# Kernel tuning notes

Measured on AMD Instinct MI355X. Metric: run time of the kernel, lower is better.

Reference implementation:

```python
import jax, jax.numpy as jnp
import numpy as np
from jax import lax

BN_EPS = 1e-5
EYE_EPS = 1e-6
ZIP = 128
TAU = 0.2

def _cov(x):
    # x: [C, N] rows=variables, cols=observations (torch.cov semantics)
    n = x.shape[1]
    xc = x - jnp.mean(x, axis=1, keepdims=True)
    return (xc @ xc.T) / (n - 1)

def setup_inputs() -> dict:
    key = jax.random.key(0)
    ks = jax.random.split(key, 10)
    d = {}
    d["img_feats_f"] = jax.random.normal(ks[0], (1, 128, 480, 640), dtype=jnp.float32)
    d["pcd_feats_f"] = jax.random.normal(ks[1], (22432, 128), dtype=jnp.float32)
    # ConvBlock(128->128, k=3, s=1, p=1) + BatchNorm (eval) + ReLU
    d["conv_w"] = jax.random.normal(ks[2], (128, 128, 3, 3), dtype=jnp.float32) * 0.02
    d["conv_b"] = jnp.zeros((128,), dtype=jnp.float32)
    d["bn_gamma"] = jnp.ones((128,), dtype=jnp.float32)
    d["bn_beta"] = jnp.zeros((128,), dtype=jnp.float32)
    d["bn_mean"] = jnp.zeros((128,), dtype=jnp.float32)
    d["bn_var"] = jnp.ones((128,), dtype=jnp.float32)
    # Linear(128->128) + ReLU
    d["lin_w"] = jax.random.normal(ks[3], (128, 128), dtype=jnp.float32) * 0.02
    d["lin_b"] = jnp.zeros((128,), dtype=jnp.float32)
    return d

def reference(img_feats_f, pcd_feats_f, conv_w, conv_b, bn_gamma, bn_beta, bn_mean, bn_var, lin_w, lin_b):
    B, C, h, w = img_feats_f.shape
    # zip_fea_2d: Conv2d(3x3, pad 1) + BN(eval) + ReLU
    x = lax.conv_general_dilated(img_feats_f, conv_w, (1, 1), ((1, 1), (1, 1)),
                                 dimension_numbers=("NCHW", "OIHW", "NCHW"))
    x = x + conv_b[None, :, None, None]
    x = (x - bn_mean[None, :, None, None]) * (bn_gamma / jnp.sqrt(bn_var + BN_EPS))[None, :, None, None] + bn_beta[None, :, None, None]
    img_zip = jax.nn.relu(x)
    # zip_fea_3d: Linear + ReLU
    pcd_zip = jax.nn.relu(pcd_feats_f @ lin_w.T + lin_b)

    tmp_img_f = img_zip.reshape(ZIP, -1)        # [128, h*w]
    tmp_pcd_f = pcd_zip.T                        # [128, Np]
    cov_img = _cov(tmp_img_f)                    # [128, 128]
    cov_pcd = _cov(tmp_pcd_f)                    # [128, 128]

    eye = jnp.eye(ZIP, dtype=cov_img.dtype) * EYE_EPS
    sc_ip = (cov_img @ jnp.linalg.inv(cov_pcd + eye)) / ZIP
    sc_pi = (cov_pcd @ jnp.linalg.inv(cov_img + eye)) / ZIP
    at_ip = jax.nn.softmax(sc_pi, axis=-1)
    at_pi = jax.nn.softmax(sc_ip, axis=-1)
    tmp_img_fb = (at_ip @ tmp_img_f).reshape(-1, h, w)[None]   # [1,128,h,w]
    tmp_pcd_fb = (at_pi @ tmp_pcd_f).T                          # [Np,128]

    at_ii = jax.nn.softmax((cov_img @ cov_img.T) / ZIP, axis=-1)
    at_pp = jax.nn.softmax((cov_pcd @ cov_pcd.T) / ZIP, axis=-1)
    tmp_img_fa = (at_ii @ tmp_img_f).reshape(-1, h, w)[None]
    tmp_pcd_fa = (at_pp @ tmp_pcd_f).T

    img_out = (tmp_img_fb + tmp_img_fa) / 2 * TAU + img_feats_f * (1 - TAU)
    pcd_out = (tmp_pcd_fb + tmp_pcd_fa) / 2 * TAU + pcd_feats_f * (1 - TAU)
    return (img_out, pcd_out)
```

## Files before the change

### kernel.cpp

```cpp
#include <hip/hip_runtime.h>
#include <math.h>

#define HH 480
#define WW 640
#define HWSZ (HH*WW)
#define NPC 22432
#define IMG_SZ (128*HWSZ)
#define NBI 256
#define NBP 64
#define CHUNK_I 1200
#define CHUNK_P 351

typedef unsigned short u16;
typedef unsigned int u32;
typedef __attribute__((ext_vector_type(8))) short bf16x8;
typedef __attribute__((ext_vector_type(4))) float f32x4;

#define OFF_SUMS_IMG 0
#define OFF_SUMS_PCD 128
#define OFF_BIAS2    256
#define OFF_COV_IMG  512
#define OFF_COV_PCD  16896
#define OFF_INV_IMG  33280
#define OFF_INV_PCD  49664
#define OFF_MT_IMG   66048
#define OFF_MT_PCD   82432
#define OFF_LWT      98816
#define OFF_PSUMS    115200
#define OFF_MB       147968
#define OFF_WT       152064
#define OFF_PSUMS_P  OFF_WT
#define OFF_PART_IMG 299520
#define OFF_PART_PCD 4493824
#define OFF_WB       5542400
#define OFF_TIMG_F   5616128
#define TIMG_PAD_W 642
#define TIMG_PX (482*642)
#define TIMG_PLANE (TIMG_PX*32)
#define WS_NEED_FLOATS 25420544

__device__ inline u32 pack_bf16(float a, float b) {
  u32 ua = __float_as_uint(a), ub = __float_as_uint(b);
  ua += 0x7FFFu + ((ua >> 16) & 1u);
  ub += 0x7FFFu + ((ub >> 16) & 1u);
  return (ua >> 16) | (ub & 0xFFFF0000u);
}
__device__ inline u16 to_bf16(float v) {
  u32 u = __float_as_uint(v); u += 0x7FFFu + ((u >> 16) & 1u);
  return (u16)(u >> 16);
}
__device__ inline float4 f4_fnma(float4 v, float f, float4 p) {
  return make_float4(v.x - f*p.x, v.y - f*p.y, v.z - f*p.z, v.w - f*p.w);
}

__global__ void prep_kernel(const float* __restrict__ conv_w, const float* __restrict__ conv_b,
                            const float* __restrict__ gamma, const float* __restrict__ beta,
                            const float* __restrict__ mean, const float* __restrict__ var,
                            const float* __restrict__ lin_w, float* __restrict__ ws, int big) {
  int tid = blockIdx.x * blockDim.x + threadIdx.x;
  int nth = gridDim.x * blockDim.x;
  for (int oc = tid; oc < 128; oc += nth) {
    float s = gamma[oc] / sqrtf(var[oc] + 1e-5f);
    ws[OFF_BIAS2 + oc] = (conv_b[oc] - mean[oc]) * s + beta[oc];
  }
  if (big) {
    u16* Wf = (u16*)(ws + OFF_WB);
    for (int e = tid; e < 9*128*128; e += nth) {
      int j = e & 7, l = (e >> 3) & 63, ob = (e >> 9) & 7;
      int ci32 = (e >> 12) & 3, tap = e >> 14;
      int oc = ob*16 + (l & 15);
      int ci = ci32*32 + ((l >> 4) & 3)*8 + j;
      float s = gamma[oc] / sqrtf(var[oc] + 1e-5f);
      Wf[e] = to_bf16(conv_w[(oc*128 + ci)*9 + tap] * s);
    }
  } else {
    for (int e = tid; e < 128*9*128; e += nth) {
      int oc = e & 127; int k = (e >> 7) % 9; int ci = e / 1152;
      float s = gamma[oc] / sqrtf(var[oc] + 1e-5f);
      ws[OFF_WT + e] = conv_w[(oc*128 + ci)*9 + k] * s;
    }
  }
  for (int e = tid; e < 128*128; e += nth) {
    int c2 = e & 127; int k = e >> 7;
    ws[OFF_LWT + e] = lin_w[c2*128 + k];
  }
}

__launch_bounds__(256)
__global__ void timg_kernel(const float* __restrict__ img, u16* __restrict__ Timg) {
  __shared__ float xt[64][133];
  const int b = blockIdx.x;
  const int t = threadIdx.x;
  if (b >= 4800) {
    int tid = (b - 4800) * 256 + t;
    if (tid < (642*2 + 480*2) * 16) {
      int px = tid >> 4, u = tid & 15;
      int q = u >> 2, j = u & 3;
      int addr;
      if (px < 642) addr = px;
      else if (px < 1284) addr = 481*642 + (px - 642);
      else if (px < 1764) addr = (px - 1284 + 1) * 642;
      else addr = (px - 1764 + 1) * 642 + 641;
      ((uint4*)Timg)[(size_t)q*(TIMG_PX*4) + (size_t)addr*4 + j] = make_uint4(0u,0u,0u,0u);
    }
    return;
  }
  const int h = b / 10, w0 = (b % 10) * 64;
  const int wq = t & 15, cg = t >> 4;
#pragma unroll
  for (int i = 0; i < 8; ++i) {
    int ci = cg + i*16;
    float4 v = *(const float4*)&img[(size_t)ci*HWSZ + h*WW + w0 + wq*4];
    xt[wq*4+0][ci] = v.x; xt[wq*4+1][ci] = v.y;
    xt[wq*4+2][ci] = v.z; xt[wq*4+3][ci] = v.w;
  }
  __syncthreads();
  const int wp = t >> 2, q = t & 3, c0 = q * 32;
  u32 out[16];
#pragma unroll
  for (int j = 0; j < 16; ++j) {
    float a = xt[wp][c0 + 2*j], bb = xt[wp][c0 + 2*j + 1];
    out[j] = pack_bf16(a, bb);
  }
  u16* dst = Timg + (size_t)q*TIMG_PLANE
           + ((size_t)(h+1)*TIMG_PAD_W + (w0 + 1 + wp)) * 32;
#pragma unroll
  for (int qq = 0; qq < 4; ++qq)
    *(uint4*)(dst + qq*8) = make_uint4(out[qq*4], out[qq*4+1], out[qq*4+2], out[qq*4+3]);
}

#define REG_ROWS 6
#define REG_COLS 66
#define REG_PX (REG_ROWS*REG_COLS)
__launch_bounds__(256, 2)
__global__ void conv_mfma6_kernel(const u16* __restrict__ Timg,
                                  const u16* __restrict__ Wf,
                                  const float* __restrict__ ws,
                                  float* __restrict__ X) {
  __shared__ __align__(16) u16 reg_lds[REG_PX * 44];
  const int b = blockIdx.x;
  const int h0 = (b / 10) * 4;
  const int w0 = (b % 10) * 64;
  const int t = threadIdx.x;
  const int wv = t >> 6, l = t & 63;
  const int n_lane = l & 15, k_lane = l >> 4;
  const int ocg = wv & 1;
  const int rowg = wv >> 1;

  f32x4 acc[4][8];
#pragma unroll
  for (int mt = 0; mt < 4; ++mt)
#pragma unroll
    for (int nt = 0; nt < 8; ++nt) acc[mt][nt] = (f32x4){0.f,0.f,0.f,0.f};

#pragma unroll 1
  for (int qc = 0; qc < 4; ++qc) {
    __syncthreads();
    const u16* plane = Timg + (size_t)qc * TIMG_PLANE;
    for (int e = t; e < REG_PX * 4; e += 256) {
      int px = e >> 2, j = e & 3;
      int r = px / REG_COLS, c = px - r * REG_COLS;
      const u16* src = plane + ((size_t)(h0 + r) * TIMG_PAD_W + (w0 + c)) * 32 + j*8;
      *(uint4*)((char*)reg_lds + px * 88 + j * 16) = *(const uint4*)src;
    }
    __syncthreads();
    const u16* wq = Wf + (qc*8 + ocg*4)*512 + l*8;
#pragma unroll 1
    for (int tap = 0; tap < 9; ++tap) {
      const int kh = (tap * 11) >> 5;
      const int kw = tap - kh * 3;
      const int cb = n_lane + kw;
      const int rb = rowg*2 + kh;
      const u16* wtap = wq + tap * 16384;
      bf16x8 Af[4], Bf[8];
#pragma unroll
      for (int mt = 0; mt < 4; ++mt)
        Af[mt] = *(const bf16x8*)(wtap + mt*512);
#pragma unroll
      for (int nt = 0; nt < 8; ++nt) {
        int px = (rb + (nt >> 2)) * REG_COLS + cb + (nt & 3) * 16;
        Bf[nt] = *(const bf16x8*)((char*)reg_lds + px * 88 + k_lane * 16);
      }
#pragma unroll
      for (int mt = 0; mt < 4; ++mt)
#pragma unroll
        for (int nt = 0; nt < 8; ++nt)
          acc[mt][nt] = __builtin_amdgcn_mfma_f32_16x16x32_bf16(Af[mt], Bf[nt], acc[mt][nt], 0, 0, 0);
    }
  }
  const float* bias = ws + OFF_BIAS2;
#pragma unroll
  for (int mt = 0; mt < 4; ++mt) {
    f32x4 bv = *(const f32x4*)(bias + ocg*64 + mt*16 + k_lane*4);
#pragma unroll
    for (int nt = 0; nt < 8; ++nt) {
      int row = h0 + rowg*2 + (nt >> 2);
      int col = w0 + (nt & 3)*16 + n_lane;
#pragma unroll
      for (int rr = 0; rr < 4; ++rr) {
        int oc = ocg*64 + mt*16 + k_lane*4 + rr;
        float v = acc[mt][nt][rr] + bv[rr];
        X[(size_t)oc * HWSZ + row*WW + col] = fmaxf(v, 0.f);
      }
    }
  }
}

__launch_bounds__(256)
__global__ void conv_kernel(const float* __restrict__ img,
                            const float* __restrict__ ws,
                            float* __restrict__ outX) {
  __shared__ __align__(16) float xs[8][10][20];
  __shared__ __align__(16) float wsm[8][9][64];
  const int b = blockIdx.x;
  const int oc0 = (b & 1) * 64;
  const int sidx = b >> 1;
  const int h0 = (sidx / 40) * 8;
  const int w0 = (sidx % 40) * 16;
  const int t = threadIdx.x;
  const int oc_t = t & 15;
  const int px_t = t >> 4;
  const int ph = px_t >> 1;
  const int pw0 = (px_t & 1) * 8;
  float acc[4][8];
#pragma unroll
  for (int o = 0; o < 4; o++)
#pragma unroll
    for (int m = 0; m < 8; m++) acc[o][m] = 0.f;
  const float* wT = ws + OFF_WT;
  for (int ci0 = 0; ci0 < 128; ci0 += 8) {
    __syncthreads();
    for (int e = t; e < 1440; e += 256) {
      int ci = e / 180; int rem = e - ci*180; int r = rem / 18; int cc2 = rem - r*18;
      int gh = h0 + r - 1, gw = w0 + cc2 - 1;
      float v = 0.f;
      if ((unsigned)gh < (unsigned)HH && (unsigned)gw < (unsigned)WW)
        v = img[(ci0+ci)*HWSZ + gh*WW + gw];
      xs[ci][r][cc2] = v;
    }
    for (int e = t; e < 4608; e += 256) {
      int oc = e & 63; int k = (e >> 6) % 9; int ci = e / 576;
      wsm[ci][k][oc] = wT[((ci0+ci)*9 + k)*128 + oc0 + oc];
    }
    __syncthreads();
#pragma unroll
    for (int ci = 0; ci < 8; ci++) {
#pragma unroll
      for (int kh = 0; kh < 3; kh++) {
        float x10[10];
        float4 xa = *(const float4*)&xs[ci][ph+kh][pw0];
        float4 xb = *(const float4*)&xs[ci][ph+kh][pw0+4];
        x10[0]=xa.x; x10[1]=xa.y; x10[2]=xa.z; x10[3]=xa.w;
        x10[4]=xb.x; x10[5]=xb.y; x10[6]=xb.z; x10[7]=xb.w;
        x10[8]=xs[ci][ph+kh][pw0+8]; x10[9]=xs[ci][ph+kh][pw0+9];
#pragma unroll
        for (int kw = 0; kw < 3; kw++) {
          float4 wv = *(const float4*)&wsm[ci][kh*3+kw][oc_t*4];
#pragma unroll
          for (int m = 0; m < 8; m++) {
            float xv = x10[kw+m];
            acc[0][m] += wv.x*xv; acc[1][m] += wv.y*xv;
            acc[2][m] += wv.z*xv; acc[3][m] += wv.w*xv;
          }
        }
      }
    }
  }
#pragma unroll
  for (int o = 0; o < 4; o++) {
    int oc = oc0 + oc_t*4 + o;
    float bias = ws[OFF_BIAS2 + oc];
    float4 r0, r1;
    r0.x = fmaxf(acc[o][0]+bias, 0.f); r0.y = fmaxf(acc[o][1]+bias, 0.f);
    r0.z = fmaxf(acc[o][2]+bias, 0.f); r0.w = fmaxf(acc[o][3]+bias, 0.f);
    r1.x = fmaxf(acc[o][4]+bias, 0.f); r1.y = fmaxf(acc[o][5]+bias, 0.f);
    r1.z = fmaxf(acc[o][6]+bias, 0.f); r1.w = fmaxf(acc[o][7]+bias, 0.f);
    float* dst = outX + (size_t)oc*HWSZ + (h0+ph)*WW + w0 + pw0;
    *(float4*)dst = r0; *(float4*)(dst+4) = r1;
  }
}

__launch_bounds__(256)
__global__ void linear_kernel(const float* __restrict__ pcd,
                              const float* __restrict__ ws,
                              const float* __restrict__ lin_b,
                              float* __restrict__ Z) {
  __shared__ __align__(16) float Mt[128][132];
  __shared__ __align__(16) float zs[16][132];
  const int b = blockIdx.x, t = threadIdx.x;
  const int n0 = b * 16;
#pragma unroll
  for (int i = 0; i < 16; i++) {
    int idx = t + i*256; int r = idx >> 5; int c4 = (idx & 31)*4;
    *(float4*)&Mt[r][c4] = *(const float4*)&ws[OFF_LWT + r*128 + c4];
  }
#pragma unroll
  for (int i = 0; i < 2; i++) {
    int idx = t + i*256; int r = idx >> 5; int c4 = (idx & 31)*4;
    *(float4*)&zs[r][c4] = *(const float4*)&pcd[(size_t)(n0+r)*128 + c4];
  }
  __syncthreads();
  const int nl = t & 15;
  const int c0 = (t >> 4) * 8;
  float acc[8];
#pragma unroll
  for (int q = 0; q < 8; q++) acc[q] = 0.f;
#pragma unroll 8
  for (int k = 0; k < 128; k++) {
    float z = zs[nl][k];
    float4 wa = *(const float4*)&Mt[k][c0];
    float4 wb = *(const float4*)&Mt[k][c0+4];
    acc[0]+=z*wa.x; acc[1]+=z*wa.y; acc[2]+=z*wa.z; acc[3]+=z*wa.w;
    acc[4]+=z*wb.x; acc[5]+=z*wb.y; acc[6]+=z*wb.z; acc[7]+=z*wb.w;
  }
  float4 ba = *(const float4*)&lin_b[c0];
  float4 bb = *(const float4*)&lin_b[c0+4];
  float4 r0, r1;
  r0.x = fmaxf(acc[0]+ba.x,0.f); r0.y = fmaxf(acc[1]+ba.y,0.f);
  r0.z = fmaxf(acc[2]+ba.z,0.f); r0.w = fmaxf(acc[3]+ba.w,0.f);
  r1.x = fmaxf(acc[4]+bb.x,0.f); r1.y = fmaxf(acc[5]+bb.y,0.f);
  r1.z = fmaxf(acc[6]+bb.z,0.f); r1.w = fmaxf(acc[7]+bb.w,0.f);
  float* dst = Z + (size_t)(n0+nl)*128 + c0;
  *(float4*)dst = r0; *(float4*)(dst+4) = r1;
}

__launch_bounds__(256)
__global__ void gram_img_mfma_kernel(const float* __restrict__ X,
                                     float* __restrict__ part,
                                     float* __restrict__ psums) {
  __shared__ __align__(16) u16 tile[128*64];
  const int b = blockIdx.x, t = threadIdx.x;
  const int px0 = b * CHUNK_I;
  const int pg = t & 15;
  const int g0 = t >> 4;
  const int wv = t >> 6, l = t & 63;
  const int i0 = (wv >> 1) * 64, j0 = (wv & 1) * 64;
  const int row16 = l & 15, kq = l >> 4;
  float csum[8];
#pragma unroll
  for (int q = 0; q < 8; ++q) csum[q] = 0.f;
  f32x4 acc[4][4];
#pragma unroll
  for (int a = 0; a < 4; ++a)
#pragma unroll
    for (int q = 0; q < 4; ++q) acc[a][q] = (f32x4){0.f,0.f,0.f,0.f};

  for (int ti = 0; ti < 19; ++ti) {
    const int plg = ti*64 + pg*4;
    float4 v[8];
    if (ti < 18) {
#pragma unroll
      for (int cc = 0; cc < 8; ++cc) {
        int c = g0 + cc*16;
        v[cc] = *(const float4*)(X + (size_t)c*HWSZ + px0 + plg);
      }
    } else {
#pragma unroll
      for (int cc = 0; cc < 8; ++cc) {
        int c = g0 + cc*16;
        const float* src = X + (size_t)c*HWSZ + px0;
#pragma unroll
        for (int j = 0; j < 4; ++j) {
          int p = plg + j;
          ((float*)&v[cc])[j] = (p < CHUNK_I) ? src[p] : 0.f;
        }
      }
    }
    __syncthreads();
#pragma unroll
    for (int cc = 0; cc < 8; ++cc) {
      int c = g0 + cc*16;
      csum[cc] += v[cc].x + v[cc].y + v[cc].z + v[cc].w;
      u32 w0 = pack_bf16(v[cc].x, v[cc].y);
      u32 w1 = pack_bf16(v[cc].z, v[cc].w);
      *(uint2*)((char*)tile + c*128 + ((pg*8) ^ ((c & 7) << 4))) = make_uint2(w0, w1);
    }
    __syncthreads();
#pragma unroll
    for (int f = 0; f < 2; ++f) {
      bf16x8 Af[4], Bf[4];
#pragma unroll
      for (int mt = 0; mt < 4; ++mt) {
        int c = i0 + mt*16 + row16;
        Af[mt] = *(const bf16x8*)((char*)tile + c*128 + ((f*64 + kq*16) ^ ((c & 7) << 4)));
      }
#pragma unroll
      for (int nt = 0; nt < 4; ++nt) {
        int c = j0 + nt*16 + row16;
        Bf[nt] = *(const bf16x8*)((char*)tile + c*128 + ((f*64 + kq*16) ^ ((c & 7) << 4)));
      }
#pragma unroll
      for (int mt = 0; mt < 4; ++mt)
#pragma unroll
        for (int nt = 0; nt < 4; ++nt)
          acc[mt][nt] = __builtin_amdgcn_mfma_f32_16x16x32_bf16(Af[mt], Bf[nt], acc[mt][nt], 0, 0, 0);
    }
  }
#pragma unroll
  for (int cc = 0; cc < 8; ++cc) {
    float s = csum[cc];
    s += __shfl_xor(s, 1, 64);
    s += __shfl_xor(s, 2, 64);
    s += __shfl_xor(s, 4, 64);
    s += __shfl_xor(s, 8, 64);
    if (pg == 0) psums[b*128 + g0 + cc*16] = s;
  }
  float* dst = part + (size_t)b*16384;
#pragma unroll
  for (int mt = 0; mt < 4; ++mt)
#pragma unroll
    for (int nt = 0; nt < 4; ++nt) {
#pragma unroll
      for (int r = 0; r < 4; ++r) {
        int i = i0 + mt*16 + kq*4 + r;
        int j = j0 + nt*16 + row16;
        dst[i*128 + j] = acc[mt][nt][r];
      }
    }
}

__launch_bounds__(256)
__global__ void gram_pcd_kernel(const float* __restrict__ Z, float* __restrict__ part,
                                float* __restrict__ psums_p) {
  __shared__ __align__(16) float zt[64][132];
  __shared__ float ps4[4][32][4];
  const int b = blockIdx.x, t = threadIdx.x;
  const int n0 = b * CHUNK_P;
  const int i0 = (t >> 4) * 8, j0 = (t & 15) * 8;
  float acc[8][8];
#pragma unroll
  for (int a = 0; a < 8; a++)
#pragma unroll
    for (int q = 0; q < 8; q++) acc[a][q] = 0.f;
  float fsum[4] = {0.f, 0.f, 0.f, 0.f};
  for (int tile = 0; tile < 6; tile++) {
    __syncthreads();
#pragma unroll
    for (int i = 0; i < 8; i++) {
      int idx = t + i*256; int r = idx >> 5; int c4 = (idx & 31)*4;
      int lrow = tile*64 + r;
      int n = n0 + lrow;
      float4 v = {0.f,0.f,0.f,0.f};
      if (lrow < CHUNK_P && n < NPC) v = *(const float4*)&Z[(size_t)n*128 + c4];
      *(float4*)&zt[r][c4] = v;
      fsum[0] += v.x; fsum[1] += v.y; fsum[2] += v.z; fsum[3] += v.w;
    }
    __syncthreads();
#pragma unroll 4
    for (int n = 0; n < 64; n++) {
      float4 a0 = *(const float4*)&zt[n][i0];
      float4 a1 = *(const float4*)&zt[n][i0+4];
      float4 b0 = *(const float4*)&zt[n][j0];
      float4 b1 = *(const float4*)&zt[n][j0+4];
      float av[8] = {a0.x,a0.y,a0.z,a0.w,a1.x,a1.y,a1.z,a1.w};
      float bv[8] = {b0.x,b0.y,b0.z,b0.w,b1.x,b1.y,b1.z,b1.w};
#pragma unroll
      for (int a = 0; a < 8; a++)
#pragma unroll
        for (int q = 0; q < 8; q++) acc[a][q] += av[a]*bv[q];
    }
  }
  float* dst = part + (size_t)b*16384;
#pragma unroll
  for (int a = 0; a < 8; a++) {
    float4 w0v = {acc[a][0],acc[a][1],acc[a][2],acc[a][3]};
    float4 w1v = {acc[a][4],acc[a][5],acc[a][6],acc[a][7]};
    *(float4*)&dst[(i0+a)*128 + j0] = w0v;
    *(float4*)&dst[(i0+a)*128 + j0 + 4] = w1v;
  }
  const int wv2 = t >> 6;
#pragma unroll
  for (int j2 = 0; j2 < 4; ++j2) fsum[j2] += __shfl_down(fsum[j2], 32, 64);
  if ((t & 63) < 32) {
#pragma unroll
    for (int j2 = 0; j2 < 4; ++j2) ps4[wv2][t & 31][j2] = fsum[j2];
  }
  __syncthreads();
  if (t < 128) {
    float s = ps4[0][t>>2][t&3] + ps4[1][t>>2][t&3]
            + ps4[2][t>>2][t&3] + ps4[3][t>>2][t&3];
    psums_p[b*128 + t] = s;
  }
}

__launch_bounds__(128)
__global__ void reduce_cov_kernel(float* __restrict__ ws) {
  const int b = blockIdx.x, t = threadIdx.x;
  const bool isimg = (b < 128);
  const int i = isimg ? b : b - 128;
  const int nparts = isimg ? NBI : NBP;
  const float* part = ws + (isimg ? OFF_PART_IMG : OFF_PART_PCD);
  __shared__ float sums[128];
  if (isimg) {
    const float* ps = ws + OFF_PSUMS;
    float s = 0.f;
    for (int p = 0; p < NBI; ++p) s += ps[p*128 + t];
    sums[t] = s;
  } else {
    const float* psp = ws + OFF_PSUMS_P;
    float s = 0.f;
    for (int p = 0; p < NBP; ++p) s += psp[p*128 + t];
    sums[t] = s;
  }
  __syncthreads();
  float g = 0.f;
  for (int p = 0; p < nparts; p++) g += part[(size_t)p*16384 + i*128 + t];
  float Si = sums[i];
  float Sj = sums[t];
  float n = isimg ? (float)HWSZ : (float)NPC;
  float cov = (g - Si*Sj/n) / (n - 1.f);
  ws[(isimg ? OFF_COV_IMG : OFF_COV_PCD) + i*128 + t] = cov;
}

__launch_bounds__(256, 1)
__global__ void invert_kernel(float* __restrict__ ws) {
  __shared__ float A_[128*132];
  __shared__ float Rb_[16*132];
  __shared__ float prw[16];
  __shared__ float pcl[16];
  const int blk = blockIdx.x, t = threadIdx.x;
  const float* src = ws + (blk == 0 ? OFF_COV_IMG : OFF_COV_PCD);
  float* dst = ws + (blk == 0 ? OFF_INV_IMG : OFF_INV_PCD);
  for (int e = t; e < 16384; e += 256) {
    int i = e >> 7, j = e & 127;
    A_[i*132 + j] = src[e] + ((i == j) ? 1e-6f : 0.f);
  }
#pragma unroll 1
  for (int p = 0; p < 8; ++p) {
    const int k0 = p * 16;
    __syncthreads();
    if (t < 64) {
      const int r = t & 15, cg = t >> 4, cb = cg * 4;
      float4 d = *(const float4*)&A_[(k0 + r)*132 + k0 + cb];
#pragma unroll 1
      for (int k = 0; k < 16; ++k) {
        const int kg = k >> 2, km = k & 3;
        if (r == k) {
          prw[cb+0] = d.x; prw[cb+1] = d.y; prw[cb+2] = d.z; prw[cb+3] = d.w;
        }
        if (cg == kg) {
          float el = (km==0) ? d.x : (km==1) ? d.y : (km==2) ? d.z : d.w;
          pcl[r] = el;
        }
        __builtin_amdgcn_wave_barrier();
        float ip = 1.f / pcl[k];
        float f  = pcl[r];
        float p0 = prw[cb+0], p1 = prw[cb+1], p2 = prw[cb+2], p3 = prw[cb+3];
        __builtin_amdgcn_wave_barrier();
        if (r == k) {
          d.x *= ip; d.y *= ip; d.z *= ip; d.w *= ip;
          if (cg == kg) { if (km==0) d.x=ip; else if (km==1) d.y=ip; else if (km==2) d.z=ip; else d.w=ip; }
        } else {
          float g = f * ip;
          d.x -= g*p0; d.y -= g*p1; d.z -= g*p2; d.w -= g*p3;
          if (cg == kg) { if (km==0) d.x=-g; else if (km==1) d.y=-g; else if (km==2) d.z=-g; else d.w=-g; }
        }
        __builtin_amdgcn_wave_barrier();
      }
      *(float4*)&Rb_[r*132 + k0 + cb] = d;
    }
    __syncthreads();
    {
      const int r = t & 15, ch = t >> 4;
      if ((ch >> 1) != p) {
        const int j0 = ch * 8;
        float4 dv0 = *(const float4*)&Rb_[r*132 + k0];
        float4 dv1 = *(const float4*)&Rb_[r*132 + k0 + 4];
        float4 dv2 = *(const float4*)&Rb_[r*132 + k0 + 8];
        float4 dv3 = *(const float4*)&Rb_[r*132 + k0 + 12];
        float dv[16] = {dv0.x,dv0.y,dv0.z,dv0.w, dv1.x,dv1.y,dv1.z,dv1.w,
                        dv2.x,dv2.y,dv2.z,dv2.w, dv3.x,dv3.y,dv3.z,dv3.w};
        float4 a0 = {0,0,0,0}, a1 = {0,0,0,0};
#pragma unroll
        for (int s = 0; s < 16; ++s) {
          float4 r0v = *(const float4*)&A_[(k0+s)*132 + j0];
          float4 r1v = *(const float4*)&A_[(k0+s)*132 + j0 + 4];
          float w = dv[s];
          a0.x += w*r0v.x; a0.y += w*r0v.y; a0.z += w*r0v.z; a0.w += w*r0v.w;
          a1.x += w*r1v.x; a1.y += w*r1v.y; a1.z += w*r1v.z; a1.w += w*r1v.w;
        }
        *(float4*)&Rb_[r*132 + j0] = a0;
        *(float4*)&Rb_[r*132 + j0 + 4] = a1;
      }
    }
    __syncthreads();
    {
      const int tr = t >> 4, tc = t & 15;
      const int r0 = tr * 8, c0 = tc * 8;
      const bool pivrow = (tr >> 1) == p;
      const bool pivcol = (tc >> 1) == p;
      float4 acc[8][2];
      float4 F4[8][4];
      if (pivrow) {
#pragma unroll
        for (int i = 0; i < 8; ++i) {
          acc[i][0] = *(const float4*)&Rb_[(r0 + i - k0)*132 + c0];
          acc[i][1] = *(const float4*)&Rb_[(r0 + i - k0)*132 + c0 + 4];
        }
      } else {
#pragma unroll
        for (int i = 0; i < 8; ++i) {
          F4[i][0] = *(const float4*)&A_[(r0+i)*132 + k0];
          F4[i][1] = *(const float4*)&A_[(r0+i)*132 + k0 + 4];
          F4[i][2] = *(const float4*)&A_[(r0+i)*132 + k0 + 8];
          F4[i][3] = *(const float4*)&A_[(r0+i)*132 + k0 + 12];
        }
        if (pivcol) {
#pragma unroll
          for (int i = 0; i < 8; ++i) {
            acc[i][0] = make_float4(0.f,0.f,0.f,0.f);
            acc[i][1] = make_float4(0.f,0.f,0.f,0.f);
          }
        } else {
#pragma unroll
          for (int i = 0; i < 8; ++i) {
            acc[i][0] = *(const float4*)&A_[(r0+i)*132 + c0];
            acc[i][1] = *(const float4*)&A_[(r0+i)*132 + c0 + 4];
          }
        }
      }
      __syncthreads();
      if (!pivrow) {
#pragma unroll
        for (int s = 0; s < 16; ++s) {
          float4 rb0 = *(const float4*)&Rb_[s*132 + c0];
          float4 rb1 = *(const float4*)&Rb_[s*132 + c0 + 4];
#pragma unroll
          for (int i = 0; i < 8; ++i) {
            float fs = (s&3)==0 ? F4[i][s>>2].x : (s&3)==1 ? F4[i][s>>2].y
                     : (s&3)==2 ? F4[i][s>>2].z : F4[i][s>>2].w;
            acc[i][0] = f4_fnma(acc[i][0], fs, rb0);
            acc[i][1] = f4_fnma(acc[i][1], fs, rb1);
          }
        }
      }
#pragma unroll
      for (int i = 0; i < 8; ++i) {
        *(float4*)&A_[(r0+i)*132 + c0]     = acc[i][0];
        *(float4*)&A_[(r0+i)*132 + c0 + 4] = acc[i][1];
      }
    }
  }
  __syncthreads();
  for (int e = t; e < 16384; e += 256)
    dst[e] = A_[(e >> 7)*132 + (e & 127)];
}

__launch_bounds__(128)
__global__ void attn_kernel(float* __restrict__ ws) {
  const int b = blockIdx.x, j = threadIdx.x;
  const bool isimg = (b < 128);
  const int i = isimg ? b : b - 128;
  const float* rowA = ws + (isimg ? OFF_COV_PCD : OFF_COV_IMG) + i*128;
  const float* matA = ws + (isimg ? OFF_INV_IMG : OFF_INV_PCD);
  const float* rowB = ws + (isimg ? OFF_COV_IMG : OFF_COV_PCD) + i*128;
  const float* matB = ws + (isimg ? OFF_COV_IMG : OFF_COV_PCD);
  __shared__ float rA[128], rB[128], red[128];
  rA[j] = rowA[j]; rB[j] = rowB[j];
  __syncthreads();
  float dA = 0.f, dB = 0.f;
#pragma unroll 8
  for (int k = 0; k < 128; ++k) {
    dA += rA[k] * matA[k*128 + j];
    dB += rB[k] * matB[k*128 + j];
  }
  dA *= 0.0078125f; dB *= 0.0078125f;
  red[j] = dA; __syncthreads();
  for (int s2 = 64; s2 > 0; s2 >>= 1) { if (j < s2) red[j] = fmaxf(red[j], red[j+s2]); __syncthreads(); }
  float mA = red[0]; __syncthreads();
  float eA = expf(dA - mA);
  red[j] = eA; __syncthreads();
  for (int s2 = 64; s2 > 0; s2 >>= 1) { if (j < s2) red[j] += red[j+s2]; __syncthreads(); }
  float sA = red[0]; __syncthreads();
  red[j] = dB; __syncthreads();
  for (int s2 = 64; s2 > 0; s2 >>= 1) { if (j < s2) red[j] = fmaxf(red[j], red[j+s2]); __syncthreads(); }
  float mB = red[0]; __syncthreads();
  float eB = expf(dB - mB);
  red[j] = eB; __syncthreads();
  for (int s2 = 64; s2 > 0; s2 >>= 1) { if (j < s2) red[j] += red[j+s2]; __syncthreads(); }
  float sB = red[0]; __syncthreads();
  float m = 0.1f * (eA/sA + eB/sB);
  if (isimg) {
    int f = j >> 5, ob = i >> 4, l = ((j >> 3) & 3)*16 + (i & 15), jj = j & 7;
    ((u16*)(ws + OFF_MB))[(f*8 + ob)*512 + l*8 + jj] = to_bf16(m);
  } else {
    ws[OFF_MT_PCD + j*128 + i] = m;
  }
}

__launch_bounds__(256, 4)
__global__ void img_final_mfma_kernel(const float* __restrict__ img_in,
                                      const float* __restrict__ ws,
                                      float* __restrict__ io) {
  __shared__ __align__(16) char smem[34816];
  u16* bt = (u16*)smem;
  float* ts = (float*)smem;
  const int blk = blockIdx.x, t = threadIdx.x;
  const int px0 = blk * 128;
  const int pxg = (t & 31) * 4;
  const int cp0 = t >> 5;
#pragma unroll
  for (int cc = 0; cc < 8; ++cc) {
    int cpair = cp0 + cc*8;
    const float* s0 = io + (size_t)(2*cpair)*HWSZ + px0 + pxg;
    float4 a = *(const float4*)s0;
    float4 b4 = *(const float4*)(s0 + HWSZ);
#pragma unroll
    for (int j = 0; j < 4; ++j) {
      int pxl = pxg + j;
      *(u32*)((char*)bt + pxl*256 + ((cpair*4) ^ ((pxl & 7) << 4))) =
          pack_bf16(((const float*)&a)[j], ((const float*)&b4)[j]);
    }
  }
  __syncthreads();
  const int wv = t >> 6, l = t & 63;
  const int i0 = (wv >> 1) * 64, j0 = (wv & 1) * 64;
  const int row16 = l & 15, kq = l >> 4;
  const u16* Mbf = (const u16*)(ws + OFF_MB);
  f32x4 acc[4][4];
#pragma unroll
  for (int a = 0; a < 4; ++a)
#pragma unroll
    for (int q = 0; q < 4; ++q) acc[a][q] = (f32x4){0.f,0.f,0.f,0.f};
#pragma unroll
  for (int f = 0; f < 4; ++f) {
    bf16x8 Bf[4], Am[4];
#pragma unroll
    for (int nt = 0; nt < 4; ++nt) {
      int pxl = j0 + nt*16 + row16;
      Bf[nt] = *(const bf16x8*)((char*)bt + pxl*256 + ((f*64 + kq*16) ^ ((pxl & 7) << 4)));
    }
#pragma unroll
    for (int mt = 0; mt < 4; ++mt) {
      int ob = (wv >> 1) * 4 + mt;
      Am[mt] = *(const bf16x8*)(Mbf + (f*8 + ob)*512 + l*8);
    }
#pragma unroll
    for (int mt = 0; mt < 4; ++mt)
#pragma unroll
      for (int nt = 0; nt < 4; ++nt)
        acc[mt][nt] = __builtin_amdgcn_mfma_f32_16x16x32_bf16(Am[mt], Bf[nt], acc[mt][nt], 0, 0, 0);
  }
#pragma unroll 1
  for (int half = 0; half < 2; ++half) {
    __syncthreads();
    if ((wv & 1) == half) {
#pragma unroll
      for (int mt = 0; mt < 4; ++mt)
#pragma unroll
        for (int nt = 0; nt < 4; ++nt) {
          int lpx = nt*16 + row16;
#pragma unroll
          for (int r = 0; r < 4; ++r) {
            int c = i0 + mt*16 + kq*4 + r;
            ts[c*68 + lpx] = acc[mt][nt][r];
          }
        }
    }
    __syncthreads();
    const int cq = t >> 2, p4 = (t & 3) * 4;
#pragma unroll
    for (int cp = 0; cp < 2; ++cp) {
      int c = cp*64 + cq;
#pragma unroll
      for (int j = 0; j < 4; ++j) {
        int lpx = p4 + j*16;
        float4 v = *(const float4*)&ts[c*68 + lpx];
        size_t off = (size_t)c*HWSZ + px0 + half*64 + lpx;
        float4 o = *(const float4*)&img_in[off];
        float4 r;
        r.x = v.x + 0.8f*o.x; r.y = v.y + 0.8f*o.y;
        r.z = v.z + 0.8f*o.z; r.w = v.w + 0.8f*o.w;
        *(float4*)&io[off] = r;
      }
    }
  }
}

__launch_bounds__(256)
__global__ void pcd_final_kernel(const float* __restrict__ pcd_in,
                                 const float* __restrict__ ws,
                                 float* __restrict__ Z) {
  __shared__ __align__(16) float Mt[128][132];
  __shared__ __align__(16) float zs[16][132];
  const int b = blockIdx.x, t = threadIdx.x;
  const int n0 = b * 16;
#pragma unroll
  for (int i = 0; i < 16; i++) {
    int idx = t + i*256; int r = idx >> 5; int c4 = (idx & 31)*4;
    *(float4*)&Mt[r][c4] = *(const float4*)&ws[OFF_MT_PCD + r*128 + c4];
  }
#pragma unroll
  for (int i = 0; i < 2; i++) {
    int idx = t + i*256; int r = idx >> 5; int c4 = (idx & 31)*4;
    *(float4*)&zs[r][c4] = *(const float4*)&Z[(size_t)(n0+r)*128 + c4];
  }
  __syncthreads();
  const int nl = t & 15;
  const int c0 = (t >> 4) * 8;
  float acc[8];
#pragma unroll
  for (int q = 0; q < 8; q++) acc[q] = 0.f;
#pragma unroll 8
  for (int k = 0; k < 128; k++) {
    float z = zs[nl][k];
    float4 wa = *(const float4*)&Mt[k][c0];
    float4 wb = *(const float4*)&Mt[k][c0+4];
    acc[0]+=z*wa.x; acc[1]+=z*wa.y; acc[2]+=z*wa.z; acc[3]+=z*wa.w;
    acc[4]+=z*wb.x; acc[5]+=z*wb.y; acc[6]+=z*wb.z; acc[7]+=z*wb.w;
  }
  size_t off = (size_t)(n0+nl)*128 + c0;
  float4 pa = *(const float4*)&pcd_in[off];
  float4 pb = *(const float4*)&pcd_in[off+4];
  float4 r0, r1;
  r0.x = acc[0] + 0.8f*pa.x; r0.y = acc[1] + 0.8f*pa.y;
  r0.z = acc[2] + 0.8f*pa.z; r0.w = acc[3] + 0.8f*pa.w;
  r1.x = acc[4] + 0.8f*pb.x; r1.y = acc[5] + 0.8f*pb.y;
  r1.z = acc[6] + 0.8f*pb.z; r1.w = acc[7] + 0.8f*pb.w;
  *(float4*)&Z[off] = r0; *(float4*)&Z[off+4] = r1;
}

extern "C" void kernel_launch(void* const* d_in, const int* in_sizes, int n_in,
                              void* d_out, int out_size, void* d_ws, size_t ws_size,
                              hipStream_t stream) {
  (void)in_sizes; (void)n_in; (void)out_size;
  const float* img_in = (const float*)d_in[0];
  const float* pcd_in = (const float*)d_in[1];
  const float* conv_w = (const float*)d_in[2];
  const float* conv_b = (const float*)d_in[3];
  const float* gamma  = (const float*)d_in[4];
  const float* beta   = (const float*)d_in[5];
  const float* mean   = (const float*)d_in[6];
  const float* var    = (const float*)d_in[7];
  const float* lin_w  = (const float*)d_in[8];
  const float* lin_b  = (const float*)d_in[9];
  float* out = (float*)d_out;
  float* X = out;
  float* Z = out + IMG_SZ;
  float* ws = (float*)d_ws;
  const int big = (ws_size >= (size_t)WS_NEED_FLOATS * 4) ? 1 : 0;

  hipLaunchKernelGGL(prep_kernel, dim3(64), dim3(256), 0, stream,
                     conv_w, conv_b, gamma, beta, mean, var, lin_w, ws, big);
  if (big) {
    u16* Timg = (u16*)(ws + OFF_TIMG_F);
    u16* Wf = (u16*)(ws + OFF_WB);
    hipLaunchKernelGGL(timg_kernel, dim3(4941), dim3(256), 0, stream, img_in, Timg);
    hipLaunchKernelGGL(conv_mfma6_kernel, dim3(1200), dim3(256), 0, stream, Timg, Wf, ws, X);
  } else {
    hipLaunchKernelGGL(conv_kernel, dim3(4800), dim3(256), 0, stream, img_in, ws, X);
  }
  hipLaunchKernelGGL(linear_kernel, dim3(NPC/16), dim3(256), 0, stream, pcd_in, ws, lin_b, Z);
  hipLaunchKernelGGL(gram_img_mfma_kernel, dim3(NBI), dim3(256), 0, stream,
                     X, ws + OFF_PART_IMG, ws + OFF_PSUMS);
  hipLaunchKernelGGL(gram_pcd_kernel, dim3(NBP), dim3(256), 0, stream,
                     Z, ws + OFF_PART_PCD, ws + OFF_PSUMS_P);
  hipLaunchKernelGGL(reduce_cov_kernel, dim3(256), dim3(128), 0, stream, ws);
  hipLaunchKernelGGL(invert_kernel, dim3(2), dim3(256), 0, stream, ws);
  hipLaunchKernelGGL(attn_kernel, dim3(256), dim3(128), 0, stream, ws);
  hipLaunchKernelGGL(img_final_mfma_kernel, dim3(HWSZ/128), dim3(256), 0, stream, img_in, ws, X);
  hipLaunchKernelGGL(pcd_final_kernel, dim3(NPC/16), dim3(256), 0, stream, pcd_in, ws, Z);
}
```

Measured before the change: 577.8 us.

## Store conv activations as bf16 intermediate and read it in gram and final kernels

When workspace is large enough, the conv epilogue writes the ReLU output as bf16 into a workspace buffer instead of fp32 into the output. The gram and final-mix kernels then read this half-size buffer, which cuts global memory traffic for the 157 MB activation tensor by half on two read passes and one write pass. Column sums are now computed from bf16-rounded values, which slightly changes mean precision. The path only runs if the harness provides about 180 MB of workspace, so it may be inactive.

```diff
diff --git a/kernel.cpp b/kernel.cpp
--- a/kernel.cpp
+++ b/kernel.cpp
@@ -38,6 +38,8 @@
 #define TIMG_PX (482*642)
 #define TIMG_PLANE (TIMG_PX*32)
 #define WS_NEED_FLOATS 25420544
+#define OFF_XB       25420544
+#define WS_NEED2_FLOATS 45081344
 
 __device__ inline u32 pack_bf16(float a, float b) {
   u32 ua = __float_as_uint(a), ub = __float_as_uint(b);
@@ -48,6 +50,9 @@
 __device__ inline u16 to_bf16(float v) {
   u32 u = __float_as_uint(v); u += 0x7FFFu + ((u >> 16) & 1u);
   return (u16)(u >> 16);
+}
+__device__ inline float from_bf16(u16 v) {
+  return __uint_as_float(((u32)v) << 16);
 }
 __device__ inline float4 f4_fnma(float4 v, float f, float4 p) {
   return make_float4(v.x - f*p.x, v.y - f*p.y, v.z - f*p.z, v.w - f*p.w);
@@ -136,7 +141,8 @@
 __global__ void conv_mfma6_kernel(const u16* __restrict__ Timg,
                                   const u16* __restrict__ Wf,
                                   const float* __restrict__ ws,
-                                  float* __restrict__ X) {
+                                  float* __restrict__ X,
+                                  u16* __restrict__ xb) {
   __shared__ __align__(16) u16 reg_lds[REG_PX * 44];
   const int b = blockIdx.x;
   const int h0 = (b / 10) * 4;
@@ -189,18 +195,36 @@
     }
   }
   const float* bias = ws + OFF_BIAS2;
-#pragma unroll
-  for (int mt = 0; mt < 4; ++mt) {
-    f32x4 bv = *(const f32x4*)(bias + ocg*64 + mt*16 + k_lane*4);
-#pragma unroll
-    for (int nt = 0; nt < 8; ++nt) {
-      int row = h0 + rowg*2 + (nt >> 2);
-      int col = w0 + (nt & 3)*16 + n_lane;
-#pragma unroll
-      for (int rr = 0; rr < 4; ++rr) {
-        int oc = ocg*64 + mt*16 + k_lane*4 + rr;
-        float v = acc[mt][nt][rr] + bv[rr];
-        X[(size_t)oc * HWSZ + row*WW + col] = fmaxf(v, 0.f);
+  if (xb) {
+#pragma unroll
+    for (int mt = 0; mt < 4; ++mt) {
+      f32x4 bv = *(const f32x4*)(bias + ocg*64 + mt*16 + k_lane*4);
+#pragma unroll
+      for (int nt = 0; nt < 8; ++nt) {
+        int row = h0 + rowg*2 + (nt >> 2);
+        int col = w0 + (nt & 3)*16 + n_lane;
+#pragma unroll
+        for (int rr = 0; rr < 4; ++rr) {
+          int oc = ocg*64 + mt*16 + k_lane*4 + rr;
+          float v = acc[mt][nt][rr] + bv[rr];
+          xb[(size_t)oc * HWSZ + row*WW + col] = to_bf16(fmaxf(v, 0.f));
+        }
+      }
+    }
+  } else {
+#pragma unroll
+    for (int mt = 0; mt < 4; ++mt) {
+      f32x4 bv = *(const f32x4*)(bias + ocg*64 + mt*16 + k_lane*4);
+#pragma unroll
+      for (int nt = 0; nt < 8; ++nt) {
+        int row = h0 + rowg*2 + (nt >> 2);
+        int col = w0 + (nt & 3)*16 + n_lane;
+#pragma unroll
+        for (int rr = 0; rr < 4; ++rr) {
+          int oc = ocg*64 + mt*16 + k_lane*4 + rr;
+          float v = acc[mt][nt][rr] + bv[rr];
+          X[(size_t)oc * HWSZ + row*WW + col] = fmaxf(v, 0.f);
+        }
       }
     }
   }
@@ -249,9 +273,9 @@
       for (int kh = 0; kh < 3; kh++) {
         float x10[10];
         float4 xa = *(const float4*)&xs[ci][ph+kh][pw0];
-        float4 xb = *(const float4*)&xs[ci][ph+kh][pw0+4];
+        float4 xb2 = *(const float4*)&xs[ci][ph+kh][pw0+4];
         x10[0]=xa.x; x10[1]=xa.y; x10[2]=xa.z; x10[3]=xa.w;
-        x10[4]=xb.x; x10[5]=xb.y; x10[6]=xb.z; x10[7]=xb.w;
+        x10[4]=xb2.x; x10[5]=xb2.y; x10[6]=xb2.z; x10[7]=xb2.w;
         x10[8]=xs[ci][ph+kh][pw0+8]; x10[9]=xs[ci][ph+kh][pw0+9];
 #pragma unroll
         for (int kw = 0; kw < 3; kw++) {
@@ -326,16 +350,18 @@
 
 __launch_bounds__(256)
 __global__ void gram_img_mfma_kernel(const float* __restrict__ X,
+                                     const u16* __restrict__ xb,
                                      float* __restrict__ part,
                                      float* __restrict__ psums) {
   __shared__ __align__(16) u16 tile[128*64];
   const int b = blockIdx.x, t = threadIdx.x;
   const int px0 = b * CHUNK_I;
-  const int pg = t & 15;
-  const int g0 = t >> 4;
   const int wv = t >> 6, l = t & 63;
   const int i0 = (wv >> 1) * 64, j0 = (wv & 1) * 64;
   const int row16 = l & 15, kq = l >> 4;
+  const int pg = t & 15;
+  const int g0 = t >> 4;
+  const int cb16 = t >> 1, hb16 = t & 1;
   float csum[8];
 #pragma unroll
   for (int q = 0; q < 8; ++q) csum[q] = 0.f;
@@ -346,34 +372,56 @@
     for (int q = 0; q < 4; ++q) acc[a][q] = (f32x4){0.f,0.f,0.f,0.f};
 
   for (int ti = 0; ti < 19; ++ti) {
-    const int plg = ti*64 + pg*4;
-    float4 v[8];
-    if (ti < 18) {
+    if (xb) {
+      uint4 v[4];
+#pragma unroll
+      for (int gi = 0; gi < 4; ++gi) {
+        int g = hb16*4 + gi;
+        int plg = ti*64 + g*8;
+        if (plg < CHUNK_I)
+          v[gi] = *(const uint4*)(xb + (size_t)cb16*HWSZ + px0 + plg);
+        else
+          v[gi] = make_uint4(0u,0u,0u,0u);
+      }
+      __syncthreads();
+#pragma unroll
+      for (int gi = 0; gi < 4; ++gi) {
+        int g = hb16*4 + gi;
+        *(uint4*)((char*)tile + cb16*128 + ((g*16) ^ ((cb16 & 7) << 4))) = v[gi];
+        const u16* p16 = (const u16*)&v[gi];
+#pragma unroll
+        for (int j = 0; j < 8; ++j) csum[0] += from_bf16(p16[j]);
+      }
+    } else {
+      const int plg = ti*64 + pg*4;
+      float4 v[8];
+      if (ti < 18) {
+#pragma unroll
+        for (int cc = 0; cc < 8; ++cc) {
+          int c = g0 + cc*16;
+          v[cc] = *(const float4*)(X + (size_t)c*HWSZ + px0 + plg);
+        }
+      } else {
+#pragma unroll
+        for (int cc = 0; cc < 8; ++cc) {
+          int c = g0 + cc*16;
+          const float* src = X + (size_t)c*HWSZ + px0;
+#pragma unroll
+          for (int j = 0; j < 4; ++j) {
+            int p = plg + j;
+            ((float*)&v[cc])[j] = (p < CHUNK_I) ? src[p] : 0.f;
+          }
+        }
+      }
+      __syncthreads();
 #pragma unroll
       for (int cc = 0; cc < 8; ++cc) {
         int c = g0 + cc*16;
-        v[cc] = *(const float4*)(X + (size_t)c*HWSZ + px0 + plg);
-      }
-    } else {
-#pragma unroll
-      for (int cc = 0; cc < 8; ++cc) {
-        int c = g0 + cc*16;
-        const float* src = X + (size_t)c*HWSZ + px0;
-#pragma unroll
-        for (int j = 0; j < 4; ++j) {
-          int p = plg + j;
-          ((float*)&v[cc])[j] = (p < CHUNK_I) ? src[p] : 0.f;
-        }
-      }
-    }
-    __syncthreads();
-#pragma unroll
-    for (int cc = 0; cc < 8; ++cc) {
-      int c = g0 + cc*16;
-      csum[cc] += v[cc].x + v[cc].y + v[cc].z + v[cc].w;
-      u32 w0 = pack_bf16(v[cc].x, v[cc].y);
-      u32 w1 = pack_bf16(v[cc].z, v[cc].w);
-      *(uint2*)((char*)tile + c*128 + ((pg*8) ^ ((c & 7) << 4))) = make_uint2(w0, w1);
+        csum[cc] += v[cc].x + v[cc].y + v[cc].z + v[cc].w;
+        u32 w0 = pack_bf16(v[cc].x, v[cc].y);
+        u32 w1 = pack_bf16(v[cc].z, v[cc].w);
+        *(uint2*)((char*)tile + c*128 + ((pg*8) ^ ((c & 7) << 4))) = make_uint2(w0, w1);
+      }
     }
     __syncthreads();
 #pragma unroll
@@ -395,15 +443,22 @@
         for (int nt = 0; nt < 4; ++nt)
           acc[mt][nt] = __builtin_amdgcn_mfma_f32_16x16x32_bf16(Af[mt], Bf[nt], acc[mt][nt], 0, 0, 0);
     }
-  }
-#pragma unroll
-  for (int cc = 0; cc < 8; ++cc) {
-    float s = csum[cc];
+    __syncthreads();
+  }
+  if (xb) {
+    float s = csum[0];
     s += __shfl_xor(s, 1, 64);
-    s += __shfl_xor(s, 2, 64);
-    s += __shfl_xor(s, 4, 64);
-    s += __shfl_xor(s, 8, 64);
-    if (pg == 0) psums[b*128 + g0 + cc*16] = s;
+    if ((t & 1) == 0) psums[b*128 + cb16] = s;
+  } else {
+#pragma unroll
+    for (int cc = 0; cc < 8; ++cc) {
+      float s = csum[cc];
+      s += __shfl_xor(s, 1, 64);
+      s += __shfl_xor(s, 2, 64);
+      s += __shfl_xor(s, 4, 64);
+      s += __shfl_xor(s, 8, 64);
+      if (pg == 0) psums[b*128 + g0 + cc*16] = s;
+    }
   }
   float* dst = part + (size_t)b*16384;
 #pragma unroll
@@ -691,6 +746,7 @@
 __launch_bounds__(256, 4)
 __global__ void img_final_mfma_kernel(const float* __restrict__ img_in,
                                       const float* __restrict__ ws,
+                                      const u16* __restrict__ xb,
                                       float* __restrict__ io) {
   __shared__ __align__(16) char smem[34816];
   u16* bt = (u16*)smem;
@@ -699,17 +755,37 @@
   const int px0 = blk * 128;
   const int pxg = (t & 31) * 4;
   const int cp0 = t >> 5;
-#pragma unroll
-  for (int cc = 0; cc < 8; ++cc) {
-    int cpair = cp0 + cc*8;
-    const float* s0 = io + (size_t)(2*cpair)*HWSZ + px0 + pxg;
-    float4 a = *(const float4*)s0;
-    float4 b4 = *(const float4*)(s0 + HWSZ);
-#pragma unroll
-    for (int j = 0; j < 4; ++j) {
-      int pxl = pxg + j;
-      *(u32*)((char*)bt + pxl*256 + ((cpair*4) ^ ((pxl & 7) << 4))) =
-          pack_bf16(((const float*)&a)[j], ((const float*)&b4)[j]);
+  if (xb) {
+#pragma unroll
+    for (int cc = 0; cc < 8; ++cc) {
+      int cpair = cp0 + cc*8;
+      const u16* s0 = xb + (size_t)(2*cpair)*HWSZ + px0 + pxg;
+      uint2 ua = *(const uint2*)s0;
+      uint2 ub = *(const uint2*)(s0 + HWSZ);
+      u32 w[4];
+      w[0] = (ua.x & 0xFFFFu) | ((ub.x & 0xFFFFu) << 16);
+      w[1] = (ua.x >> 16)     | (ub.x & 0xFFFF0000u);
+      w[2] = (ua.y & 0xFFFFu) | ((ub.y & 0xFFFFu) << 16);
+      w[3] = (ua.y >> 16)     | (ub.y & 0xFFFF0000u);
+#pragma unroll
+      for (int j = 0; j < 4; ++j) {
+        int pxl = pxg + j;
+        *(u32*)((char*)bt + pxl*256 + ((cpair*4) ^ ((pxl & 7) << 4))) = w[j];
+      }
+    }
+  } else {
+#pragma unroll
+    for (int cc = 0; cc < 8; ++cc) {
+      int cpair = cp0 + cc*8;
+      const float* s0 = io + (size_t)(2*cpair)*HWSZ + px0 + pxg;
+      float4 a = *(const float4*)s0;
+      float4 b4 = *(const float4*)(s0 + HWSZ);
+#pragma unroll
+      for (int j = 0; j < 4; ++j) {
+        int pxl = pxg + j;
+        *(u32*)((char*)bt + pxl*256 + ((cpair*4) ^ ((pxl & 7) << 4))) =
+            pack_bf16(((const float*)&a)[j], ((const float*)&b4)[j]);
+      }
     }
   }
   __syncthreads();
@@ -838,7 +914,9 @@
   float* X = out;
   float* Z = out + IMG_SZ;
   float* ws = (float*)d_ws;
-  const int big = (ws_size >= (size_t)WS_NEED_FLOATS * 4) ? 1 : 0;
+  const int big  = (ws_size >= (size_t)WS_NEED_FLOATS * 4) ? 1 : 0;
+  const int big2 = (ws_size >= (size_t)WS_NEED2_FLOATS * 4) ? 1 : 0;
+  u16* Xb = big2 ? (u16*)(ws + OFF_XB) : (u16*)nullptr;
 
   hipLaunchKernelGGL(prep_kernel, dim3(64), dim3(256), 0, stream,
                      conv_w, conv_b, gamma, beta, mean, var, lin_w, ws, big);
@@ -846,18 +924,19 @@
     u16* Timg = (u16*)(ws + OFF_TIMG_F);
     u16* Wf = (u16*)(ws + OFF_WB);
     hipLaunchKernelGGL(timg_kernel, dim3(4941), dim3(256), 0, stream, img_in, Timg);
-    hipLaunchKernelGGL(conv_mfma6_kernel, dim3(1200), dim3(256), 0, stream, Timg, Wf, ws, X);
+    hipLaunchKernelGGL(conv_mfma6_kernel, dim3(1200), dim3(256), 0, stream, Timg, Wf, ws, X, Xb);
   } else {
     hipLaunchKernelGGL(conv_kernel, dim3(4800), dim3(256), 0, stream, img_in, ws, X);
   }
   hipLaunchKernelGGL(linear_kernel, dim3(NPC/16), dim3(256), 0, stream, pcd_in, ws, lin_b, Z);
   hipLaunchKernelGGL(gram_img_mfma_kernel, dim3(NBI), dim3(256), 0, stream,
-                     X, ws + OFF_PART_IMG, ws + OFF_PSUMS);
+                     X, Xb, ws + OFF_PART_IMG, ws + OFF_PSUMS);
   hipLaunchKernelGGL(gram_pcd_kernel, dim3(NBP), dim3(256), 0, stream,
                      Z, ws + OFF_PART_PCD, ws + OFF_PSUMS_P);
   hipLaunchKernelGGL(reduce_cov_kernel, dim3(256), dim3(128), 0, stream, ws);
   hipLaunchKernelGGL(invert_kernel, dim3(2), dim3(256), 0, stream, ws);
   hipLaunchKernelGGL(attn_kernel, dim3(256), dim3(128), 0, stream, ws);
-  hipLaunchKernelGGL(img_final_mfma_kernel, dim3(HWSZ/128), dim3(256), 0, stream, img_in, ws, X);
+  hipLaunchKernelGGL(img_final_mfma_kernel, dim3(HWSZ/128), dim3(256), 0, stream,
+                     img_in, ws, Xb, X);
   hipLaunchKernelGGL(pcd_final_kernel, dim3(NPC/16), dim3(256), 0, stream, pcd_in, ws, Z);
 }
```

Result: faster. 543.8 us (-5.9%).
